# Optimization experiments

Measured on AMD Instinct MI355X. Metric: run time of the kernel, lower is better.

Reference implementation:

```python
import jax, jax.numpy as jnp
import numpy as np

B, S, E, H = 16, 2048, 512, 64


def setup_inputs() -> dict:
    key = jax.random.key(0)
    k1, k2, k3, k4, k5 = jax.random.split(key, 5)
    inp = {
        "input": jax.random.normal(k1, (B, S, E), dtype=jnp.float32),
        "seq_lengths": jax.random.randint(k2, (B,), 0, S).astype(jnp.int64),
        "Wq": jax.random.normal(k3, (E, H), dtype=jnp.float32) * (1.0 / np.sqrt(E)),
        "Wk": jax.random.normal(k4, (E, H), dtype=jnp.float32) * (1.0 / np.sqrt(E)),
        "Wv": jax.random.normal(k5, (E, H), dtype=jnp.float32) * (1.0 / np.sqrt(E)),
    }
    return inp


def reference(input, seq_lengths, Wq, Wk, Wv):
    # Projections (bias-free Linear): [B,S,E] @ [E,H] -> [B,S,H]
    q = input @ Wq
    k = input @ Wk
    v = input @ Wv
    Sdim = input.shape[1]
    head_size = Wk.shape[-1]
    # Padding mask: position >= seq_length -> True. Zero out q and k (NOT v),
    # exactly as the torch module does with masked_fill.
    pad = (jnp.arange(Sdim)[None, :] >= seq_lengths[:, None])[:, :, None]  # [B,S,1]
    q = jnp.where(pad, 0.0, q)
    k = jnp.where(pad, 0.0, k)
    scale = 1.0 / np.sqrt(head_size).astype(np.float32)
    # Full score matrix [B,S,S] (the memory-bound intermediate)
    scores = jnp.einsum("bsh,bth->bst", q, k) * scale
    weights = jax.nn.softmax(scores, axis=-1)
    weights = jnp.where(jnp.isnan(weights), 0.0, weights)
    out = jnp.einsum("bst,bth->bsh", weights, v)  # [B,S,H]
    return out
```

## Files before the change

### kernel.cpp

```cpp
#include <hip/hip_runtime.h>
#include <hip/hip_bf16.h>

typedef __bf16 bf16;
typedef __bf16 bf16x8 __attribute__((ext_vector_type(8)));
typedef __bf16 bf16x4 __attribute__((ext_vector_type(4)));
typedef float  f32x4  __attribute__((ext_vector_type(4)));
typedef float  f32x16 __attribute__((ext_vector_type(16)));
typedef unsigned int u32x4 __attribute__((ext_vector_type(4)));

static constexpr int SDIM = 2048;
static constexpr int EDIM = 512;
static constexpr int HDIM = 64;

typedef __attribute__((address_space(1))) const void* gptr_t;
typedef __attribute__((address_space(3))) void*       lptr_t;

__device__ __forceinline__ void gl_lds16(const bf16* g, bf16* l) {
  __builtin_amdgcn_global_load_lds((gptr_t)g, (lptr_t)l, 16, 0, 0);
}

#if __has_builtin(__builtin_amdgcn_exp2f)
#define EXP2F(x) __builtin_amdgcn_exp2f(x)
#else
#define EXP2F(x) exp2f(x)
#endif

__device__ __forceinline__ bf16x8 pack8(f32x4 a, f32x4 b) {
  bf16x8 r;
  r[0] = (bf16)a[0]; r[1] = (bf16)a[1]; r[2] = (bf16)a[2]; r[3] = (bf16)a[3];
  r[4] = (bf16)b[0]; r[5] = (bf16)b[1]; r[6] = (bf16)b[2]; r[7] = (bf16)b[3];
  return r;
}

__device__ __forceinline__ unsigned cvtpk_bf16(float a, float b) {
  unsigned r;
  asm("v_cvt_pk_bf16_f32 %0, %1, %2" : "=v"(r) : "v"(a), "v"(b));
  return r;
}

__global__ __launch_bounds__(256) void wt_kernel(const float* __restrict__ Wq,
                                                 const float* __restrict__ Wk,
                                                 const float* __restrict__ Wv,
                                                 bf16* __restrict__ Wt) {
  __shared__ float lds[64][65];
  const int mat = blockIdx.x >> 3;
  const int et  = blockIdx.x & 7;
  const float* W = (mat == 0) ? Wq : ((mat == 1) ? Wk : Wv);
  const float scale = (mat == 0) ? 0.18033688f : 1.0f;
  const int t  = threadIdx.x;
  const int er = t >> 2;
  const int c4 = (t & 3) * 16;
#pragma unroll
  for (int j = 0; j < 4; ++j) {
    f32x4 v = *(const f32x4*)(W + (size_t)(et * 64 + er) * HDIM + c4 + j * 4);
    lds[er][c4 + j * 4 + 0] = v[0]; lds[er][c4 + j * 4 + 1] = v[1];
    lds[er][c4 + j * 4 + 2] = v[2]; lds[er][c4 + j * 4 + 3] = v[3];
  }
  __syncthreads();
  const int h  = t >> 2;
  const int ec = (t & 3) * 16;
  bf16x8 o0, o1;
#pragma unroll
  for (int j = 0; j < 8; ++j) o0[j] = (bf16)(lds[ec + j][h] * scale);
#pragma unroll
  for (int j = 0; j < 8; ++j) o1[j] = (bf16)(lds[ec + 8 + j][h] * scale);
  bf16* dst = Wt + mat * (HDIM * EDIM) + (size_t)h * EDIM + et * 64 + ec;
  *(bf16x8*)dst = o0;
  *(bf16x8*)(dst + 8) = o1;
}

__global__ __launch_bounds__(256) void proj_kernel(const float* __restrict__ x,
                                                   const bf16* __restrict__ Wt,
                                                   const int* __restrict__ lens,
                                                   bf16* __restrict__ qo,
                                                   bf16* __restrict__ ko,
                                                   bf16* __restrict__ vT) {
  __shared__ __align__(16) bf16 wbuf[2][192 * 64];
  const int tid  = threadIdx.x;
  const int wave = tid >> 6;
  const int lane = tid & 63;
  const int quad = lane >> 4;
  const int l16  = lane & 15;
  const int rowbase = blockIdx.x * 64 + wave * 16;
  const int b = blockIdx.x >> 5;
  const float* xrow = x + (size_t)(rowbase + l16) * EDIM + quad * 8;
  const int srow   = lane >> 3;
  const int schunk = (lane & 7) ^ srow;

  #define WSTAGE(ck, buf) { _Pragma("unroll")                                  \
    for (int i6 = 0; i6 < 6; ++i6) {                                           \
      const int R0 = (wave * 6 + i6) * 8;                                      \
      gl_lds16(Wt + (size_t)(R0 + srow) * EDIM + (ck) * 64 + schunk * 8,       \
               &(buf)[R0 * 64]); } }

  f32x4 acc[3][4];
#pragma unroll
  for (int m = 0; m < 3; ++m)
#pragma unroll
    for (int nt = 0; nt < 4; ++nt) acc[m][nt] = (f32x4){0.f, 0.f, 0.f, 0.f};

  #define WCOMPUTE(buf, eo4, afrag) { _Pragma("unroll")                        \
    for (int m = 0; m < 3; ++m) { _Pragma("unroll")                            \
      for (int nt = 0; nt < 4; ++nt) {                                         \
        bf16x8 bfv = *(const bf16x8*)(&(buf)[(m * 64 + nt * 16 + l16) * 64 +   \
                                             ((((eo4) + quad) ^ (l16 & 7)) * 8)]); \
        acc[m][nt] = __builtin_amdgcn_mfma_f32_16x16x32_bf16(afrag, bfv, acc[m][nt], 0, 0, 0); } } }

  WSTAGE(0, wbuf[0]);
  __builtin_amdgcn_sched_barrier(0);
  f32x4 c0 = *(const f32x4*)(xrow);
  f32x4 c1 = *(const f32x4*)(xrow + 4);
  f32x4 c2 = *(const f32x4*)(xrow + 32);
  f32x4 c3 = *(const f32x4*)(xrow + 36);
  f32x4 n0 = *(const f32x4*)(xrow + 64);
  f32x4 n1 = *(const f32x4*)(xrow + 68);
  f32x4 n2 = *(const f32x4*)(xrow + 96);
  f32x4 n3 = *(const f32x4*)(xrow + 100);
  __builtin_amdgcn_sched_barrier(0);
  asm volatile("s_waitcnt vmcnt(8)" ::: "memory");
  __builtin_amdgcn_s_barrier();
  __builtin_amdgcn_sched_barrier(0);

#pragma unroll
  for (int ck = 0; ck < 8; ++ck) {
    const int cs = (ck < 7) ? (ck + 1) : 7;
    WSTAGE(cs, wbuf[(ck + 1) & 1]);
    __builtin_amdgcn_sched_barrier(0);
    const int kf = (ck < 6) ? (ck + 2) : 7;
    f32x4 m0 = *(const f32x4*)(xrow + kf * 64);
    f32x4 m1 = *(const f32x4*)(xrow + kf * 64 + 4);
    f32x4 m2 = *(const f32x4*)(xrow + kf * 64 + 32);
    f32x4 m3 = *(const f32x4*)(xrow + kf * 64 + 36);
    __builtin_amdgcn_sched_barrier(0);
    bf16x8 a = pack8(c0, c1);
    WCOMPUTE(wbuf[ck & 1], 0, a);
    a = pack8(c2, c3);
    WCOMPUTE(wbuf[ck & 1], 4, a);
    c0 = n0; c1 = n1; c2 = n2; c3 = n3;
    n0 = m0; n1 = m1; n2 = m2; n3 = m3;
    asm volatile("s_waitcnt vmcnt(4)" ::: "memory");
    __builtin_amdgcn_s_barrier();
    __builtin_amdgcn_sched_barrier(0);
  }

  int odd_or = 0;
#pragma unroll
  for (int i = 1; i < 16; i += 2) odd_or |= lens[i];
  const int len = (odd_or == 0) ? lens[2 * b] : lens[b];

#pragma unroll
  for (int nt = 0; nt < 4; ++nt) {
    const int h = nt * 16 + l16;
    bf16x4 vv;
#pragma unroll
    for (int r = 0; r < 4; ++r) {
      const int row = rowbase + quad * 4 + r;
      const int s = row & (SDIM - 1);
      const bool pad = (s >= len);
      qo[(size_t)row * HDIM + h] = (bf16)(pad ? 0.f : acc[0][nt][r]);
      ko[(size_t)row * HDIM + h] = (bf16)(pad ? 0.f : acc[1][nt][r]);
      vv[r] = (bf16)acc[2][nt][r];
    }
    *(bf16x4*)(vT + ((size_t)b * HDIM + h) * SDIM + (rowbase & (SDIM - 1)) + quad * 4) = vv;
  }
  #undef WSTAGE
  #undef WCOMPUTE
}

__global__ __launch_bounds__(256) void attn_kernel(const bf16* __restrict__ qb,
                                                   const bf16* __restrict__ kb,
                                                   const bf16* __restrict__ vT,
                                                   float* __restrict__ out) {
  __shared__ __align__(16) bf16 Kbuf[2][2][64 * 64];
  __shared__ __align__(16) bf16 Vbuf[2][2][64 * 64];
  const int tid  = threadIdx.x;
  const int wave = tid >> 6;
  const int lane = tid & 63;
  const int hi   = lane >> 5;
  const int l32  = lane & 31;
  const int iq   = wave & 1;
  const int jk   = wave >> 1;
  const int xcd = blockIdx.x & 7;
  const int jj  = blockIdx.x >> 3;
  const int b   = xcd * 2 + (jj >> 5);
  const int qbase = (jj & 31) * 64 + iq * 32;
  const bf16* q0 = qb + (size_t)b * SDIM * HDIM;
  const bf16* k0 = kb + (size_t)b * SDIM * HDIM;
  const bf16* v0 = vT + (size_t)b * HDIM * SDIM;
  const int srow   = lane >> 3;
  const int schunk = (lane & 7) ^ srow;
  const int rswz   = (l32 & 7) << 4;

  bf16x8 qf[4];
#pragma unroll
  for (int c = 0; c < 4; ++c)
    qf[c] = *(const bf16x8*)(q0 + (size_t)(qbase + l32) * HDIM + c * 16 + hi * 8);

  f32x16 O[2];
#pragma unroll
  for (int ht = 0; ht < 2; ++ht)
#pragma unroll
    for (int r = 0; r < 16; ++r) O[ht][r] = 0.f;
  float l_acc = 0.f;

  #define STAGE(sidx, db) {                                                    \
    const int key0_ = (wave & 1) * 1024 + (sidx) * 64;                         \
    if (wave < 2) {                                                            \
      const bf16* gk = k0 + (size_t)(key0_ + srow) * HDIM + schunk * 8;        \
      bf16* lk = &Kbuf[db][wave & 1][0];                                       \
      _Pragma("unroll")                                                        \
      for (int r8 = 0; r8 < 2; ++r8)                                           \
        { gl_lds16(gk + (size_t)r8 * 32 * HDIM, lk + r8 * 32 * 64);            \
          gl_lds16(gk + (size_t)(r8 * 32 + 8) * HDIM, lk + (r8 * 32 + 8) * 64);\
          gl_lds16(gk + (size_t)(r8 * 32 + 16) * HDIM, lk + (r8 * 32 + 16) * 64);\
          gl_lds16(gk + (size_t)(r8 * 32 + 24) * HDIM, lk + (r8 * 32 + 24) * 64); } \
    } else {                                                                   \
      const bf16* gv = v0 + (size_t)srow * SDIM + key0_ + schunk * 8;          \
      bf16* lv = &Vbuf[db][wave & 1][0];                                       \
      _Pragma("unroll")                                                        \
      for (int r8 = 0; r8 < 8; ++r8)                                           \
        gl_lds16(gv + (size_t)r8 * 8 * SDIM, lv + r8 * 8 * 64);                \
    }                                                                          \
  }

  STAGE(0, 0);
#pragma unroll 2
  for (int s = 0; s < 16; ++s) {
    __syncthreads();
    if (s + 1 < 16) STAGE(s + 1, (s + 1) & 1);
    const bf16* KB = &Kbuf[s & 1][jk][0];
    const bf16* VB = &Vbuf[s & 1][jk][0];

    bf16x8 pa[4];
#pragma unroll
    for (int kt = 0; kt < 2; ++kt) {
      f32x16 st;
#pragma unroll
      for (int r = 0; r < 16; ++r) st[r] = 0.f;
      const int krow = kt * 32 + l32;
      __builtin_amdgcn_s_setprio(1);
#pragma unroll
      for (int c = 0; c < 4; ++c) {
        bf16x8 kf = *(const bf16x8*)((const char*)KB + krow * 128 +
                                     ((c * 32 + hi * 16) ^ rswz));
        st = __builtin_amdgcn_mfma_f32_32x32x16_bf16(kf, qf[c], st, 0, 0, 0);
      }
      __builtin_amdgcn_s_setprio(0);
      float p[16];
#pragma unroll
      for (int r = 0; r < 16; ++r) p[r] = EXP2F(st[r]);
      float s0 = (p[0] + p[1]) + (p[2] + p[3]);
      float s1 = (p[4] + p[5]) + (p[6] + p[7]);
      float s2 = (p[8] + p[9]) + (p[10] + p[11]);
      float s3 = (p[12] + p[13]) + (p[14] + p[15]);
      l_acc += (s0 + s1) + (s2 + s3);
      unsigned u0 = cvtpk_bf16(p[0], p[1]);
      unsigned u1 = cvtpk_bf16(p[2], p[3]);
      unsigned u2 = cvtpk_bf16(p[4], p[5]);
      unsigned u3 = cvtpk_bf16(p[6], p[7]);
      asm("v_permlane32_swap_b32 %0, %1" : "+v"(u0), "+v"(u2));
      asm("v_permlane32_swap_b32 %0, %1" : "+v"(u1), "+v"(u3));
      union { u32x4 u; bf16x8 v; } f0;
      f0.u[0] = u0; f0.u[1] = u1; f0.u[2] = u2; f0.u[3] = u3;
      pa[kt * 2 + 0] = f0.v;
      unsigned u4 = cvtpk_bf16(p[8],  p[9]);
      unsigned u5 = cvtpk_bf16(p[10], p[11]);
      unsigned u6 = cvtpk_bf16(p[12], p[13]);
      unsigned u7 = cvtpk_bf16(p[14], p[15]);
      asm("v_permlane32_swap_b32 %0, %1" : "+v"(u4), "+v"(u6));
      asm("v_permlane32_swap_b32 %0, %1" : "+v"(u5), "+v"(u7));
      union { u32x4 u; bf16x8 v; } f1;
      f1.u[0] = u4; f1.u[1] = u5; f1.u[2] = u6; f1.u[3] = u7;
      pa[kt * 2 + 1] = f1.v;
    }
#pragma unroll
    for (int ht = 0; ht < 2; ++ht) {
      const int vrow = ht * 32 + l32;
      __builtin_amdgcn_s_setprio(1);
#pragma unroll
      for (int tc = 0; tc < 4; ++tc) {
        bf16x8 vf = *(const bf16x8*)((const char*)VB + vrow * 128 +
                                     ((tc * 32 + hi * 16) ^ rswz));
        O[ht] = __builtin_amdgcn_mfma_f32_32x32x16_bf16(pa[tc], vf, O[ht], 0, 0, 0);
      }
      __builtin_amdgcn_s_setprio(0);
    }
  }

  l_acc += __shfl_xor(l_acc, 32);

  float* cb = (float*)&Kbuf[0][0][0];
  float* cl = (float*)&Vbuf[0][0][0];
  __syncthreads();
  if (jk == 1) {
#pragma unroll
    for (int ht = 0; ht < 2; ++ht)
#pragma unroll
      for (int r = 0; r < 16; ++r) {
        const int qrow = (r & 3) + 8 * (r >> 2) + 4 * hi;
        cb[(iq * 32 + qrow) * 64 + ht * 32 + l32] = O[ht][r];
      }
    if (hi == 0) cl[iq * 32 + l32] = l_acc;
  }
  __syncthreads();
  if (jk == 0) {
    const float inv_own = 1.0f / (l_acc + cl[iq * 32 + l32]);
#pragma unroll
    for (int r = 0; r < 16; ++r) {
      const int qrow = (r & 3) + 8 * (r >> 2) + 4 * hi;
      const float inv = __shfl(inv_own, qrow);
#pragma unroll
      for (int ht = 0; ht < 2; ++ht) {
        const float val = (O[ht][r] + cb[(iq * 32 + qrow) * 64 + ht * 32 + l32]) * inv;
        out[((size_t)b * SDIM + qbase + qrow) * HDIM + ht * 32 + l32] = val;
      }
    }
  }
  #undef STAGE
}

extern "C" void kernel_launch(void* const* d_in, const int* in_sizes, int n_in,
                              void* d_out, int out_size, void* d_ws, size_t ws_size,
                              hipStream_t stream) {
  (void)in_sizes; (void)n_in; (void)out_size; (void)ws_size;
  const float* x  = (const float*)d_in[0];
  const int*   sl = (const int*)d_in[1];
  const float* Wq = (const float*)d_in[2];
  const float* Wk = (const float*)d_in[3];
  const float* Wv = (const float*)d_in[4];
  float* out = (float*)d_out;

  char* ws = (char*)d_ws;
  bf16* Wt = (bf16*)(ws);
  bf16* qb = (bf16*)(ws + (256 << 10));
  bf16* kb = (bf16*)(ws + (256 << 10) + (4 << 20));
  bf16* vT = (bf16*)(ws + (256 << 10) + (8 << 20));

  wt_kernel  <<<24,  256, 0, stream>>>(Wq, Wk, Wv, Wt);
  proj_kernel<<<512, 256, 0, stream>>>(x, Wt, sl, qb, kb, vT);
  attn_kernel<<<512, 256, 0, stream>>>(qb, kb, vT, out);
}
```

Measured before the change: 135.8 us.

## Split attention key tiles across 8 waves per block instead of 4

The attention block grows from 256 to 512 threads. Each wave now handles one 32-key sub-tile per step instead of two, which splits the QK and PV MFMA work four ways per query tile. K/V staging is spread across all eight waves. The final reduction merges four partial outputs and row sums through LDS, reusing the K/V buffers. This raises per-CU wave parallelism to hide exp and LDS latency, at the cost of more LDS reads of V per unit of work, a larger cross-wave reduction, and register-limit pressure from launch_bounds(512,4).

Result: no change. 133.3 us, median of 2 (-1.8%).

```diff
diff --git a/kernel.cpp b/kernel.cpp
--- a/kernel.cpp
+++ b/kernel.cpp
@@ -167,10 +167,10 @@
   #undef WCOMPUTE
 }
 
-__global__ __launch_bounds__(256) void attn_kernel(const bf16* __restrict__ qb,
-                                                   const bf16* __restrict__ kb,
-                                                   const bf16* __restrict__ vT,
-                                                   float* __restrict__ out) {
+__global__ __launch_bounds__(512, 4) void attn_kernel(const bf16* __restrict__ qb,
+                                                      const bf16* __restrict__ kb,
+                                                      const bf16* __restrict__ vT,
+                                                      float* __restrict__ out) {
   __shared__ __align__(16) bf16 Kbuf[2][2][64 * 64];
   __shared__ __align__(16) bf16 Vbuf[2][2][64 * 64];
   const int tid  = threadIdx.x;
@@ -179,7 +179,8 @@
   const int hi   = lane >> 5;
   const int l32  = lane & 31;
   const int iq   = wave & 1;
-  const int jk   = wave >> 1;
+  const int jk   = (wave >> 1) & 1;
+  const int sub  = wave >> 2;
   const int xcd = blockIdx.x & 7;
   const int jj  = blockIdx.x >> 3;
   const int b   = xcd * 2 + (jj >> 5);
@@ -204,22 +205,21 @@
   float l_acc = 0.f;
 
   #define STAGE(sidx, db) {                                                    \
-    const int key0_ = (wave & 1) * 1024 + (sidx) * 64;                         \
-    if (wave < 2) {                                                            \
-      const bf16* gk = k0 + (size_t)(key0_ + srow) * HDIM + schunk * 8;        \
-      bf16* lk = &Kbuf[db][wave & 1][0];                                       \
+    const int half_ = (wave >> 1) & 1;                                         \
+    const int rb_   = (wave & 1) * 32;                                         \
+    const int key0_ = half_ * 1024 + (sidx) * 64;                              \
+    if (wave < 4) {                                                            \
+      const bf16* gk = k0 + (size_t)(key0_ + rb_ + srow) * HDIM + schunk * 8;  \
+      bf16* lk = &Kbuf[db][half_][rb_ * 64];                                   \
       _Pragma("unroll")                                                        \
-      for (int r8 = 0; r8 < 2; ++r8)                                           \
-        { gl_lds16(gk + (size_t)r8 * 32 * HDIM, lk + r8 * 32 * 64);            \
-          gl_lds16(gk + (size_t)(r8 * 32 + 8) * HDIM, lk + (r8 * 32 + 8) * 64);\
-          gl_lds16(gk + (size_t)(r8 * 32 + 16) * HDIM, lk + (r8 * 32 + 16) * 64);\
-          gl_lds16(gk + (size_t)(r8 * 32 + 24) * HDIM, lk + (r8 * 32 + 24) * 64); } \
+      for (int j4 = 0; j4 < 4; ++j4)                                           \
+        gl_lds16(gk + (size_t)j4 * 8 * HDIM, lk + j4 * 8 * 64);                \
     } else {                                                                   \
-      const bf16* gv = v0 + (size_t)srow * SDIM + key0_ + schunk * 8;          \
-      bf16* lv = &Vbuf[db][wave & 1][0];                                       \
+      const bf16* gv = v0 + (size_t)(rb_ + srow) * SDIM + key0_ + schunk * 8;  \
+      bf16* lv = &Vbuf[db][half_][rb_ * 64];                                   \
       _Pragma("unroll")                                                        \
-      for (int r8 = 0; r8 < 8; ++r8)                                           \
-        gl_lds16(gv + (size_t)r8 * 8 * SDIM, lv + r8 * 8 * 64);                \
+      for (int j4 = 0; j4 < 4; ++j4)                                           \
+        gl_lds16(gv + (size_t)j4 * 8 * SDIM, lv + j4 * 8 * 64);                \
     }                                                                          \
   }
 
@@ -231,29 +231,30 @@
     const bf16* KB = &Kbuf[s & 1][jk][0];
     const bf16* VB = &Vbuf[s & 1][jk][0];
 
-    bf16x8 pa[4];
-#pragma unroll
-    for (int kt = 0; kt < 2; ++kt) {
-      f32x16 st;
-#pragma unroll
-      for (int r = 0; r < 16; ++r) st[r] = 0.f;
-      const int krow = kt * 32 + l32;
-      __builtin_amdgcn_s_setprio(1);
-#pragma unroll
-      for (int c = 0; c < 4; ++c) {
-        bf16x8 kf = *(const bf16x8*)((const char*)KB + krow * 128 +
-                                     ((c * 32 + hi * 16) ^ rswz));
-        st = __builtin_amdgcn_mfma_f32_32x32x16_bf16(kf, qf[c], st, 0, 0, 0);
-      }
-      __builtin_amdgcn_s_setprio(0);
-      float p[16];
-#pragma unroll
-      for (int r = 0; r < 16; ++r) p[r] = EXP2F(st[r]);
+    f32x16 st;
+#pragma unroll
+    for (int r = 0; r < 16; ++r) st[r] = 0.f;
+    const int krow = sub * 32 + l32;
+    __builtin_amdgcn_s_setprio(1);
+#pragma unroll
+    for (int c = 0; c < 4; ++c) {
+      bf16x8 kf = *(const bf16x8*)((const char*)KB + krow * 128 +
+                                   ((c * 32 + hi * 16) ^ rswz));
+      st = __builtin_amdgcn_mfma_f32_32x32x16_bf16(kf, qf[c], st, 0, 0, 0);
+    }
+    __builtin_amdgcn_s_setprio(0);
+    float p[16];
+#pragma unroll
+    for (int r = 0; r < 16; ++r) p[r] = EXP2F(st[r]);
+    {
       float s0 = (p[0] + p[1]) + (p[2] + p[3]);
       float s1 = (p[4] + p[5]) + (p[6] + p[7]);
       float s2 = (p[8] + p[9]) + (p[10] + p[11]);
       float s3 = (p[12] + p[13]) + (p[14] + p[15]);
       l_acc += (s0 + s1) + (s2 + s3);
+    }
+    bf16x8 pa0, pa1;
+    {
       unsigned u0 = cvtpk_bf16(p[0], p[1]);
       unsigned u1 = cvtpk_bf16(p[2], p[3]);
       unsigned u2 = cvtpk_bf16(p[4], p[5]);
@@ -262,7 +263,7 @@
       asm("v_permlane32_swap_b32 %0, %1" : "+v"(u1), "+v"(u3));
       union { u32x4 u; bf16x8 v; } f0;
       f0.u[0] = u0; f0.u[1] = u1; f0.u[2] = u2; f0.u[3] = u3;
-      pa[kt * 2 + 0] = f0.v;
+      pa0 = f0.v;
       unsigned u4 = cvtpk_bf16(p[8],  p[9]);
       unsigned u5 = cvtpk_bf16(p[10], p[11]);
       unsigned u6 = cvtpk_bf16(p[12], p[13]);
@@ -271,47 +272,56 @@
       asm("v_permlane32_swap_b32 %0, %1" : "+v"(u5), "+v"(u7));
       union { u32x4 u; bf16x8 v; } f1;
       f1.u[0] = u4; f1.u[1] = u5; f1.u[2] = u6; f1.u[3] = u7;
-      pa[kt * 2 + 1] = f1.v;
-    }
+      pa1 = f1.v;
+    }
+    __builtin_amdgcn_s_setprio(1);
 #pragma unroll
     for (int ht = 0; ht < 2; ++ht) {
       const int vrow = ht * 32 + l32;
-      __builtin_amdgcn_s_setprio(1);
-#pragma unroll
-      for (int tc = 0; tc < 4; ++tc) {
-        bf16x8 vf = *(const bf16x8*)((const char*)VB + vrow * 128 +
-                                     ((tc * 32 + hi * 16) ^ rswz));
-        O[ht] = __builtin_amdgcn_mfma_f32_32x32x16_bf16(pa[tc], vf, O[ht], 0, 0, 0);
-      }
-      __builtin_amdgcn_s_setprio(0);
-    }
+      bf16x8 vf0 = *(const bf16x8*)((const char*)VB + vrow * 128 +
+                                    ((sub * 64 + 0 * 32 + hi * 16) ^ rswz));
+      O[ht] = __builtin_amdgcn_mfma_f32_32x32x16_bf16(pa0, vf0, O[ht], 0, 0, 0);
+      bf16x8 vf1 = *(const bf16x8*)((const char*)VB + vrow * 128 +
+                                    ((sub * 64 + 1 * 32 + hi * 16) ^ rswz));
+      O[ht] = __builtin_amdgcn_mfma_f32_32x32x16_bf16(pa1, vf1, O[ht], 0, 0, 0);
+    }
+    __builtin_amdgcn_s_setprio(0);
   }
 
   l_acc += __shfl_xor(l_acc, 32);
 
-  float* cb = (float*)&Kbuf[0][0][0];
-  float* cl = (float*)&Vbuf[0][0][0];
+  const int grp = wave >> 1;
   __syncthreads();
-  if (jk == 1) {
-#pragma unroll
-    for (int ht = 0; ht < 2; ++ht)
-#pragma unroll
-      for (int r = 0; r < 16; ++r) {
-        const int qrow = (r & 3) + 8 * (r >> 2) + 4 * hi;
-        cb[(iq * 32 + qrow) * 64 + ht * 32 + l32] = O[ht][r];
-      }
-    if (hi == 0) cl[iq * 32 + l32] = l_acc;
+  if (grp != 0) {
+    float* pb = (grp == 1) ? (float*)&Kbuf[0][0][0]
+              : (grp == 2) ? (float*)&Kbuf[1][0][0]
+                           : (float*)&Vbuf[0][0][0];
+#pragma unroll
+    for (int r = 0; r < 16; ++r) {
+      const int qrow = (r & 3) + 8 * (r >> 2) + 4 * hi;
+      pb[(iq * 32 + qrow) * 64 + 0 * 32 + l32] = O[0][r];
+      pb[(iq * 32 + qrow) * 64 + 1 * 32 + l32] = O[1][r];
+    }
+    if (hi == 0)
+      ((float*)&Vbuf[1][0][0])[(grp - 1) * 64 + iq * 32 + l32] = l_acc;
   }
   __syncthreads();
-  if (jk == 0) {
-    const float inv_own = 1.0f / (l_acc + cl[iq * 32 + l32]);
+  if (grp == 0) {
+    const float* p1 = (const float*)&Kbuf[0][0][0];
+    const float* p2 = (const float*)&Kbuf[1][0][0];
+    const float* p3 = (const float*)&Vbuf[0][0][0];
+    const float* lp = (const float*)&Vbuf[1][0][0];
+    const float lt = l_acc + lp[0 * 64 + iq * 32 + l32]
+                   + lp[1 * 64 + iq * 32 + l32] + lp[2 * 64 + iq * 32 + l32];
+    const float inv_own = 1.0f / lt;
 #pragma unroll
     for (int r = 0; r < 16; ++r) {
       const int qrow = (r & 3) + 8 * (r >> 2) + 4 * hi;
       const float inv = __shfl(inv_own, qrow);
 #pragma unroll
       for (int ht = 0; ht < 2; ++ht) {
-        const float val = (O[ht][r] + cb[(iq * 32 + qrow) * 64 + ht * 32 + l32]) * inv;
+        const int idx = (iq * 32 + qrow) * 64 + ht * 32 + l32;
+        const float val = (O[ht][r] + p1[idx] + p2[idx] + p3[idx]) * inv;
         out[((size_t)b * SDIM + qbase + qrow) * HDIM + ht * 32 + l32] = val;
       }
     }
@@ -338,5 +348,5 @@
 
   wt_kernel  <<<24,  256, 0, stream>>>(Wq, Wk, Wv, Wt);
   proj_kernel<<<512, 256, 0, stream>>>(x, Wt, sl, qb, kb, vT);
-  attn_kernel<<<512, 256, 0, stream>>>(qb, kb, vT, out);
-}
+  attn_kernel<<<512, 512, 0, stream>>>(qb, kb, vT, out);
+}
```
